# Kernel optimization log

Measured on AMD Instinct MI355X. Metric: run time of the kernel, lower is better.

The kernel has to match this reference:

```python
import jax, jax.numpy as jnp
import numpy as np

B, S, D, NH = 4, 1000, 1024, 16
DK = D // NH  # 64
NEG_INF = -jnp.inf


def setup_inputs() -> dict:
    key = jax.random.key(0)
    ks = jax.random.split(key, 12)
    sc = 1.0 / np.sqrt(D)
    inp = {
        'q': jax.random.normal(ks[0], (B, S, D), jnp.float32),
        'k': jax.random.normal(ks[1], (B, S, D), jnp.float32),
        'v': jax.random.normal(ks[2], (B, S, D), jnp.float32),
        'mask': jnp.ones((B, S), jnp.int32),
        'Wq': jax.random.normal(ks[3], (D, D), jnp.float32) * sc,
        'bq': jax.random.normal(ks[4], (D,), jnp.float32) * sc,
        'Wk': jax.random.normal(ks[5], (D, D), jnp.float32) * sc,
        'bk': jax.random.normal(ks[6], (D,), jnp.float32) * sc,
        'Wv': jax.random.normal(ks[7], (D, D), jnp.float32) * sc,
        'bv': jax.random.normal(ks[8], (D,), jnp.float32) * sc,
        'Wp': jax.random.normal(ks[9], (D, D), jnp.float32) * sc,
        'bp': jax.random.normal(ks[10], (D,), jnp.float32) * sc,
    }
    return inp


def _split_heads(x):
    # [B, S, D] -> [B, NH, S, DK]
    b, s, _ = x.shape
    return x.reshape(b, s, NH, DK).transpose(0, 2, 1, 3)


def reference(q, k, v, mask, Wq, bq, Wk, bk, Wv, bv, Wp, bp):
    # nn.Linear: y = x @ W.T + b
    Q = _split_heads(q @ Wq.T + bq)
    K = _split_heads(k @ Wk.T + bk)
    V = _split_heads(v @ Wv.T + bv)
    # scores: [B, NH, Sq, Sk]
    S_ = jnp.einsum('bhqd,bhkd->bhqk', Q, K) / jnp.sqrt(jnp.float32(DK))
    # padding mask: [B, 1, 1, Sk]
    S_ = jnp.where(mask[:, None, None, :] == 0, NEG_INF, S_)
    # causal mask (registered tril buffer sliced to [Sq, Sk])
    sq, sk = S_.shape[2], S_.shape[3]
    causal = jnp.tril(jnp.ones((sq, sk), jnp.float32))
    S_ = jnp.where(causal == 0, NEG_INF, S_)
    A = jax.nn.softmax(S_, axis=-1)  # dropout p=0 -> identity
    # context: [B, NH, Sq, DK] -> [B, Sq, D]
    x = jnp.einsum('bhqk,bhkd->bhqd', A, V).transpose(0, 2, 1, 3)
    x = x.reshape(x.shape[0], x.shape[1], -1)
    x = x @ Wp.T + bp
    return (x, A)
```

## Files before the change

kernel.cpp:

```cpp
#include <hip/hip_runtime.h>

typedef unsigned short u16;
typedef unsigned int u32;
typedef __bf16 bf16x8 __attribute__((ext_vector_type(8)));
typedef float f32x4 __attribute__((ext_vector_type(4)));
typedef u16   u16x8 __attribute__((ext_vector_type(8)));

__device__ __forceinline__ u16 f2bf(float f) {
  __bf16 b = (__bf16)f;
  return __builtin_bit_cast(u16, b);
}
__device__ __forceinline__ float bf2f(u16 u) {
  unsigned int x = ((unsigned int)u) << 16;
  return __builtin_bit_cast(float, x);
}

__device__ __forceinline__ void gll16(const u16* g, u16* l) {
  __builtin_amdgcn_global_load_lds(
      (const __attribute__((address_space(1))) void*)g,
      (__attribute__((address_space(3))) void*)l, 16, 0, 0);
}

__global__ __launch_bounds__(256) void convall_kernel(
    const float* __restrict__ s0, const float* __restrict__ s1,
    const float* __restrict__ s2, const float* __restrict__ s3,
    const float* __restrict__ s4, const float* __restrict__ s5,
    const float* __restrict__ s6,
    u16* __restrict__ o0, u16* __restrict__ o1, u16* __restrict__ o2,
    u16* __restrict__ o3, u16* __restrict__ o4, u16* __restrict__ o5,
    u16* __restrict__ o6)
{
  const int z = blockIdx.z;
  const float* s = (z == 0) ? s0 : (z == 1) ? s1 : (z == 2) ? s2 :
                   (z == 3) ? s3 : (z == 4) ? s4 : (z == 5) ? s5 : s6;
  u16* o = (z == 0) ? o0 : (z == 1) ? o1 : (z == 2) ? o2 :
           (z == 3) ? o3 : (z == 4) ? o4 : (z == 5) ? o5 : o6;
  const long n = (z < 4) ? (1l << 20) : 4096000l;
  const long i = ((long)blockIdx.x * 256 + threadIdx.x) * 8;
  if (i >= n) return;
  f32x4 a = *(const f32x4*)(s + i);
  f32x4 b = *(const f32x4*)(s + i + 4);
  u16x8 r;
#pragma unroll
  for (int e = 0; e < 4; ++e) { r[e] = f2bf(a[e]); r[e + 4] = f2bf(b[e]); }
  *(u16x8*)(o + i) = r;
}

template<int BM, int OUT_F32>
__global__ __launch_bounds__(256, 3) void gemm_swz(
    const u16* __restrict__ A0, const u16* __restrict__ A1, const u16* __restrict__ A2,
    const u16* __restrict__ B0, const u16* __restrict__ B1, const u16* __restrict__ B2,
    const float* __restrict__ g0, const float* __restrict__ g1, const float* __restrict__ g2,
    void* __restrict__ C0, void* __restrict__ C1, void* __restrict__ C2, int Mvalid)
{
  constexpr int ACH = BM / 32;
  constexpr int MI  = BM / 32;
  const int z = blockIdx.z;
  const u16* Ab = (z == 0) ? A0 : (z == 1) ? A1 : A2;
  const u16* Bw = (z == 0) ? B0 : (z == 1) ? B1 : B2;
  const float* bias = (z == 0) ? g0 : (z == 1) ? g1 : g2;
  void* Cout = (z == 0) ? C0 : (z == 1) ? C1 : C2;

  __shared__ __align__(16) u16 As[BM * 64];
  __shared__ __align__(16) u16 Bs[128 * 64];

  const int tid = threadIdx.x;
  const int wid = tid >> 6, lane = tid & 63, ln = lane & 15, lg = lane >> 4;
  const int row0 = blockIdx.x * BM, col0 = blockIdx.y * 128;
  const int wr = (wid >> 1) * (BM / 2), wc = (wid & 1) * 64;
  const int lr8 = lane >> 3;
  const int kslot = 8 * ((lane & 7) ^ lr8);

  f32x4 acc[MI][4] = {};

  for (int kt = 0; kt < 16; ++kt) {
    const int k0 = kt * 64;
    __syncthreads();
#pragma unroll
    for (int c = 0; c < ACH; ++c) {
      int base = wid * (8 * ACH) + c * 8;
      long gr = row0 + base + lr8; if (gr >= Mvalid) gr = Mvalid - 1;
      gll16(Ab + gr * 1024 + k0 + kslot, &As[base * 64]);
    }
#pragma unroll
    for (int c = 0; c < 4; ++c) {
      int base = wid * 32 + c * 8;
      gll16(Bw + (long)(col0 + base + lr8) * 1024 + k0 + kslot, &Bs[base * 64]);
    }
    __syncthreads();

#pragma unroll
    for (int kk = 0; kk < 64; kk += 32) {
      bf16x8 af[MI], bfr[4];
#pragma unroll
      for (int i = 0; i < MI; ++i) {
        int r = wr + i * 16 + ln;
        af[i] = *(const bf16x8*)&As[r * 64 + ((kk + 8 * lg) ^ ((r & 7) << 3))];
      }
#pragma unroll
      for (int j = 0; j < 4; ++j) {
        int r = wc + j * 16 + ln;
        bfr[j] = *(const bf16x8*)&Bs[r * 64 + ((kk + 8 * lg) ^ ((r & 7) << 3))];
      }
#pragma unroll
      for (int i = 0; i < MI; ++i)
#pragma unroll
        for (int j = 0; j < 4; ++j)
          acc[i][j] = __builtin_amdgcn_mfma_f32_16x16x32_bf16(af[i], bfr[j], acc[i][j], 0, 0, 0);
    }
  }

  float bj[4];
#pragma unroll
  for (int j = 0; j < 4; ++j) bj[j] = bias[col0 + wc + j * 16 + ln];
#pragma unroll
  for (int i = 0; i < MI; ++i)
#pragma unroll
    for (int j = 0; j < 4; ++j)
#pragma unroll
      for (int reg = 0; reg < 4; ++reg) {
        int r = row0 + wr + i * 16 + 4 * lg + reg;
        int c = col0 + wc + j * 16 + ln;
        if (r < Mvalid) {
          float v = acc[i][j][reg] + bj[j];
          if constexpr (OUT_F32) ((float*)Cout)[(long)r * 1024 + c] = v;
          else                   ((u16*)Cout)[(long)r * 1024 + c] = f2bf(v);
        }
      }
}

__global__ __launch_bounds__(256) void MaskedMultiheadAttention_51591147160164_kernel(
    const u16* __restrict__ Qb, const u16* __restrict__ Kb,
    const u16* __restrict__ Vb, const int* __restrict__ maskp,
    float* __restrict__ Aout, u16* __restrict__ ctx, float* __restrict__ dumpf)
{
  __shared__ __align__(16) u16 QsPs[64 * 72];
  __shared__ __align__(16) u16 Ks[2][64 * 64];
  __shared__ __align__(16) u16 Vs[64 * 72];
  __shared__ __align__(16) float Bf[1024];

  const int bh = blockIdx.y;
  const int b = bh >> 4, h = bh & 15;
  const int tid = threadIdx.x;
  const int wid = tid >> 6, lane = tid & 63, ln = lane & 15, lg = lane >> 4;

  {
    f32x4 bv;
#pragma unroll
    for (int e = 0; e < 4; ++e) {
      int ki = tid * 4 + e;
      int mv = (ki < 1000) ? maskp[b * 1000 + ki] : 0;
      bv[e] = mv ? 0.f : -1.0e30f;
    }
    *(f32x4*)&Bf[tid * 4] = bv;
  }

  const int lr8 = lane >> 3;
  const int kslot = 8 * ((lane & 7) ^ lr8);
  const long rowb = (long)b * 1000;
  const int vr = tid >> 2, vseg = tid & 3;

  for (int half = 0; half < 2; ++half) {
    const int qb = half ? (15 - blockIdx.x) : blockIdx.x;
    const int q0 = qb * 64;
    const int nkt = qb + 1;
    const int q = q0 + wid * 16 + ln;

    __syncthreads();
#pragma unroll
    for (int p = 0; p < 2; ++p) {
      int idx = p * 256 + tid;
      int r = idx >> 3, u = idx & 7;
      int tok = q0 + r; if (tok > 999) tok = 999;
      *(u16x8*)&QsPs[r * 72 + u * 8] =
          *(const u16x8*)(Qb + (long)(b * 1000 + tok) * 1024 + h * 64 + u * 8);
    }
    __syncthreads();

    bf16x8 qf0, qf1;
    {
      int r = wid * 16 + ln;
      qf0 = *(const bf16x8*)&QsPs[r * 72 +      8 * lg];
      qf1 = *(const bf16x8*)&QsPs[r * 72 + 32 + 8 * lg];
    }
    __syncthreads();

    auto stageK = [&](int buf, int kt) {
#pragma unroll
      for (int c = 0; c < 2; ++c) {
        int r = wid * 16 + c * 8;
        gll16(Kb + (rowb + kt * 64 + r + lr8) * 1024 + h * 64 + kslot, &Ks[buf][r * 64]);
      }
    };
    auto loadV = [&](int kt, u16x8& ra, u16x8& rb) {
      const u16* s = Vb + (rowb + kt * 64 + vr) * 1024 + h * 64 + vseg * 16;
      ra = *(const u16x8*)s; rb = *(const u16x8*)(s + 8);
    };
    auto writeV = [&](const u16x8& ra, const u16x8& rb) {
#pragma unroll
      for (int e = 0; e < 8; ++e) Vs[(vseg * 16 + e) * 72 + vr] = ra[e];
#pragma unroll
      for (int e = 0; e < 8; ++e) Vs[(vseg * 16 + 8 + e) * 72 + vr] = rb[e];
    };
    auto computeS = [&](int buf, f32x4 sf[4]) {
#pragma unroll
      for (int j = 0; j < 4; ++j) {
        int r = j * 16 + ln;
        int sw = (r & 7) << 3;
        bf16x8 kf0 = *(const bf16x8*)&Ks[buf][r * 64 + ((     8 * lg) ^ sw)];
        bf16x8 kf1 = *(const bf16x8*)&Ks[buf][r * 64 + ((32 + 8 * lg) ^ sw)];
        f32x4 z = {0.f, 0.f, 0.f, 0.f};
        z = __builtin_amdgcn_mfma_f32_16x16x32_bf16(kf0, qf0, z, 0, 0, 0);
        z = __builtin_amdgcn_mfma_f32_16x16x32_bf16(kf1, qf1, z, 0, 0, 0);
        sf[j] = z;
      }
    };

    float m = -3.0e38f, l = 0.f;

    stageK(0, 0); stageK(1, 1);
    for (int t = 0; t < nkt; ++t) {
      const int buf = t & 1;
      if (t == 0 || t + 1 < nkt) asm volatile("s_waitcnt vmcnt(2)" ::: "memory");
      else                       asm volatile("s_waitcnt vmcnt(0)" ::: "memory");
      __builtin_amdgcn_sched_barrier(0);
      __builtin_amdgcn_s_barrier();

      f32x4 sf[4]; computeS(buf, sf);
      float sv[4][4];
      float smax = -3.0e38f;
#pragma unroll
      for (int j = 0; j < 4; ++j) {
        int kb = t * 64 + j * 16 + 4 * lg;
        f32x4 b4 = *(const f32x4*)&Bf[kb];
#pragma unroll
        for (int reg = 0; reg < 4; ++reg) {
          float s = sf[j][reg] * 0.125f + b4[reg];
          s = (kb + reg <= q) ? s : -1.0e30f;
          sv[j][reg] = s;
          smax = fmaxf(smax, s);
        }
      }
      smax = fmaxf(smax, __shfl_xor(smax, 16));
      smax = fmaxf(smax, __shfl_xor(smax, 32));
      float mnew = fmaxf(m, smax);
      float sum = 0.f;
#pragma unroll
      for (int j = 0; j < 4; ++j)
#pragma unroll
        for (int reg = 0; reg < 4; ++reg)
          sum += __expf(sv[j][reg] - mnew);
      sum += __shfl_xor(sum, 16);
      sum += __shfl_xor(sum, 32);
      l = l * __expf(m - mnew) + sum;
      m = mnew;
      __builtin_amdgcn_s_barrier();
      if (t + 2 < nkt) stageK(buf, t + 2);
    }

    const float rl = 1.0f / l;

    f32x4 cacc[4] = {};
    u16* Pw = &QsPs[wid * 16 * 72];

    u16x8 va0, va1, vb0, vb1;
    stageK(0, 0); loadV(0, va0, va1);
    stageK(1, 1); loadV(1, vb0, vb1);
    for (int t = 0; t < nkt; ++t) {
      const int buf = t & 1;
      if (t == 0 || t + 1 == nkt) asm volatile("s_waitcnt vmcnt(4)" ::: "memory");
      else                        asm volatile("s_waitcnt vmcnt(8)" ::: "memory");
      __builtin_amdgcn_sched_barrier(0);
      if (t & 1) writeV(vb0, vb1); else writeV(va0, va1);
      asm volatile("s_waitcnt lgkmcnt(0)" ::: "memory");
      __builtin_amdgcn_sched_barrier(0);
      __builtin_amdgcn_s_barrier();

      f32x4 sf[4]; computeS(buf, sf);
      const long arow = ((long)bh * 1000 + q) * 1000;
#pragma unroll
      for (int j = 0; j < 4; ++j) {
        int kb = t * 64 + j * 16 + 4 * lg;
        f32x4 b4 = *(const f32x4*)&Bf[kb];
        f32x4 pv4;
#pragma unroll
        for (int reg = 0; reg < 4; ++reg) {
          float s = sf[j][reg] * 0.125f + b4[reg];
          s = (kb + reg <= q) ? s : -1.0e30f;
          pv4[reg] = __expf(s - m) * rl;
        }
        float* dst = (q < 1000 && kb < 1000) ? (float*)&Aout[arow + kb]
                                             : dumpf + tid * 4;
        *(f32x4*)dst = pv4;
        u32 w0 = (u32)f2bf(pv4[0]) | ((u32)f2bf(pv4[1]) << 16);
        u32 w1 = (u32)f2bf(pv4[2]) | ((u32)f2bf(pv4[3]) << 16);
        uint2 pk; pk.x = w0; pk.y = w1;
        *(uint2*)&Pw[ln * 72 + j * 16 + 4 * lg] = pk;
      }
      asm volatile("s_waitcnt lgkmcnt(0)" ::: "memory");
      __builtin_amdgcn_sched_barrier(0);
#pragma unroll
      for (int kk = 0; kk < 64; kk += 32) {
        bf16x8 pf = *(const bf16x8*)&Pw[ln * 72 + kk + 8 * lg];
#pragma unroll
        for (int jn = 0; jn < 4; ++jn) {
          bf16x8 vf = *(const bf16x8*)&Vs[(jn * 16 + ln) * 72 + kk + 8 * lg];
          cacc[jn] = __builtin_amdgcn_mfma_f32_16x16x32_bf16(pf, vf, cacc[jn], 0, 0, 0);
        }
      }
      __builtin_amdgcn_s_barrier();
      if (t + 2 < nkt) {
        stageK(buf, t + 2);
        if (t & 1) loadV(t + 2, vb0, vb1); else loadV(t + 2, va0, va1);
      }
    }
    asm volatile("s_waitcnt vmcnt(0)" ::: "memory");

    const int qrow = q0 + wid * 16 + 4 * lg;
#pragma unroll
    for (int jn = 0; jn < 4; ++jn)
#pragma unroll
      for (int reg = 0; reg < 4; ++reg) {
        int qi = qrow + reg;
        if (qi < 1000)
          ctx[(long)(b * 1000 + qi) * 1024 + h * 64 + jn * 16 + ln] = f2bf(cacc[jn][reg]);
      }
  }
}

extern "C" void kernel_launch(void* const* d_in, const int* in_sizes, int n_in,
                              void* d_out, int out_size, void* d_ws, size_t ws_size,
                              hipStream_t stream)
{
  const float* q  = (const float*)d_in[0];
  const float* k  = (const float*)d_in[1];
  const float* v  = (const float*)d_in[2];
  const int*  msk = (const int*)d_in[3];
  const float* Wq = (const float*)d_in[4];
  const float* bq = (const float*)d_in[5];
  const float* Wk = (const float*)d_in[6];
  const float* bk = (const float*)d_in[7];
  const float* Wv = (const float*)d_in[8];
  const float* bv = (const float*)d_in[9];
  const float* Wp = (const float*)d_in[10];
  const float* bp = (const float*)d_in[11];

  u16* ws  = (u16*)d_ws;
  u16* Qc  = ws;
  u16* Kc  = ws + 4096000u;
  u16* Vc  = ws + 2u * 4096000u;
  u16* Qb  = ws + 3u * 4096000u;
  u16* Kb  = ws + 4u * 4096000u;
  u16* Vb  = ws + 5u * 4096000u;
  u16* wqb = ws + 6u * 4096000u;
  u16* wkb = wqb + (1u << 20);
  u16* wvb = wkb + (1u << 20);
  u16* wpb = wvb + (1u << 20);
  float* dumpf = (float*)(wpb + (1u << 20));
  u16* ctx = Qc;

  float* Xout = (float*)d_out;
  float* Aout = Xout + 4096000;

  convall_kernel<<<dim3(2000, 1, 7), 256, 0, stream>>>(
      Wq, Wk, Wv, Wp, q, k, v,
      wqb, wkb, wvb, wpb, Qc, Kc, Vc);
  gemm_swz<128, 0><<<dim3(32, 8, 3), 256, 0, stream>>>(
      Qc, Kc, Vc, wqb, wkb, wvb, bq, bk, bv, Qb, Kb, Vb, 4000);
  MaskedMultiheadAttention_51591147160164_kernel<<<dim3(8, 64), 256, 0, stream>>>(
      Qb, Kb, Vb, msk, Aout, ctx, dumpf);
  gemm_swz<64, 1><<<dim3(63, 8, 1), 256, 0, stream>>>(
      ctx, ctx, ctx, wpb, wpb, wpb, bp, bp, bp, Xout, Xout, Xout, 4000);
}
```

Before: 143.2 us.

## Emit V projection transposed and stage V tiles via async LDS loads

The QKV projection GEMM now writes the V output in transposed [D][tokens] layout. This lets the attention kernel stage V tiles straight into a swizzled, double-buffered LDS region with global_load_lds, the same way it already stages K. It removes the per-tile register load, the scalar transposing LDS writes and an extra lgkmcnt wait from the attention loop. The cost is a strided, uncoalesced 2-byte store epilogue for the V slice of the GEMM, plus extra LDS for the second V buffer.

```diff
diff --git a/kernel.cpp b/kernel.cpp
--- a/kernel.cpp
+++ b/kernel.cpp
@@ -51,7 +51,8 @@
     const u16* __restrict__ A0, const u16* __restrict__ A1, const u16* __restrict__ A2,
     const u16* __restrict__ B0, const u16* __restrict__ B1, const u16* __restrict__ B2,
     const float* __restrict__ g0, const float* __restrict__ g1, const float* __restrict__ g2,
-    void* __restrict__ C0, void* __restrict__ C1, void* __restrict__ C2, int Mvalid)
+    void* __restrict__ C0, void* __restrict__ C1, void* __restrict__ C2,
+    int Mvalid, int tz)
 {
   constexpr int ACH = BM / 32;
   constexpr int MI  = BM / 32;
@@ -123,20 +124,24 @@
         int c = col0 + wc + j * 16 + ln;
         if (r < Mvalid) {
           float v = acc[i][j][reg] + bj[j];
-          if constexpr (OUT_F32) ((float*)Cout)[(long)r * 1024 + c] = v;
-          else                   ((u16*)Cout)[(long)r * 1024 + c] = f2bf(v);
+          if constexpr (OUT_F32) {
+            ((float*)Cout)[(long)r * 1024 + c] = v;
+          } else {
+            if (z == tz) ((u16*)Cout)[(long)c * 4000 + r] = f2bf(v);
+            else         ((u16*)Cout)[(long)r * 1024 + c] = f2bf(v);
+          }
         }
       }
 }
 
 __global__ __launch_bounds__(256) void MaskedMultiheadAttention_51591147160164_kernel(
     const u16* __restrict__ Qb, const u16* __restrict__ Kb,
-    const u16* __restrict__ Vb, const int* __restrict__ maskp,
+    const u16* __restrict__ Vt, const int* __restrict__ maskp,
     float* __restrict__ Aout, u16* __restrict__ ctx, float* __restrict__ dumpf)
 {
   __shared__ __align__(16) u16 QsPs[64 * 72];
   __shared__ __align__(16) u16 Ks[2][64 * 64];
-  __shared__ __align__(16) u16 Vs[64 * 72];
+  __shared__ __align__(16) u16 Vs[2][64 * 64];
   __shared__ __align__(16) float Bf[1024];
 
   const int bh = blockIdx.y;
@@ -158,7 +163,6 @@
   const int lr8 = lane >> 3;
   const int kslot = 8 * ((lane & 7) ^ lr8);
   const long rowb = (long)b * 1000;
-  const int vr = tid >> 2, vseg = tid & 3;
 
   for (int half = 0; half < 2; ++half) {
     const int qb = half ? (15 - blockIdx.x) : blockIdx.x;
@@ -192,15 +196,13 @@
         gll16(Kb + (rowb + kt * 64 + r + lr8) * 1024 + h * 64 + kslot, &Ks[buf][r * 64]);
       }
     };
-    auto loadV = [&](int kt, u16x8& ra, u16x8& rb) {
-      const u16* s = Vb + (rowb + kt * 64 + vr) * 1024 + h * 64 + vseg * 16;
-      ra = *(const u16x8*)s; rb = *(const u16x8*)(s + 8);
-    };
-    auto writeV = [&](const u16x8& ra, const u16x8& rb) {
-#pragma unroll
-      for (int e = 0; e < 8; ++e) Vs[(vseg * 16 + e) * 72 + vr] = ra[e];
-#pragma unroll
-      for (int e = 0; e < 8; ++e) Vs[(vseg * 16 + 8 + e) * 72 + vr] = rb[e];
+    auto stageV = [&](int buf, int kt) {
+#pragma unroll
+      for (int c = 0; c < 2; ++c) {
+        int r = wid * 16 + c * 8;
+        gll16(Vt + (long)(h * 64 + r + lr8) * 4000 + rowb + kt * 64 + kslot,
+              &Vs[buf][r * 64]);
+      }
     };
     auto computeS = [&](int buf, f32x4 sf[4]) {
 #pragma unroll
@@ -263,16 +265,12 @@
     f32x4 cacc[4] = {};
     u16* Pw = &QsPs[wid * 16 * 72];
 
-    u16x8 va0, va1, vb0, vb1;
-    stageK(0, 0); loadV(0, va0, va1);
-    stageK(1, 1); loadV(1, vb0, vb1);
+    stageK(0, 0); stageV(0, 0);
+    stageK(1, 1); stageV(1, 1);
     for (int t = 0; t < nkt; ++t) {
       const int buf = t & 1;
       if (t == 0 || t + 1 == nkt) asm volatile("s_waitcnt vmcnt(4)" ::: "memory");
       else                        asm volatile("s_waitcnt vmcnt(8)" ::: "memory");
-      __builtin_amdgcn_sched_barrier(0);
-      if (t & 1) writeV(vb0, vb1); else writeV(va0, va1);
-      asm volatile("s_waitcnt lgkmcnt(0)" ::: "memory");
       __builtin_amdgcn_sched_barrier(0);
       __builtin_amdgcn_s_barrier();
 
@@ -304,15 +302,13 @@
         bf16x8 pf = *(const bf16x8*)&Pw[ln * 72 + kk + 8 * lg];
 #pragma unroll
         for (int jn = 0; jn < 4; ++jn) {
-          bf16x8 vf = *(const bf16x8*)&Vs[(jn * 16 + ln) * 72 + kk + 8 * lg];
+          int dr = jn * 16 + ln;
+          bf16x8 vf = *(const bf16x8*)&Vs[buf][dr * 64 + ((kk + 8 * lg) ^ ((dr & 7) << 3))];
           cacc[jn] = __builtin_amdgcn_mfma_f32_16x16x32_bf16(pf, vf, cacc[jn], 0, 0, 0);
         }
       }
       __builtin_amdgcn_s_barrier();
-      if (t + 2 < nkt) {
-        stageK(buf, t + 2);
-        if (t & 1) loadV(t + 2, vb0, vb1); else loadV(t + 2, va0, va1);
-      }
+      if (t + 2 < nkt) { stageK(buf, t + 2); stageV(buf, t + 2); }
     }
     asm volatile("s_waitcnt vmcnt(0)" ::: "memory");
 
@@ -351,7 +347,7 @@
   u16* Vc  = ws + 2u * 4096000u;
   u16* Qb  = ws + 3u * 4096000u;
   u16* Kb  = ws + 4u * 4096000u;
-  u16* Vb  = ws + 5u * 4096000u;
+  u16* Vt  = ws + 5u * 4096000u;
   u16* wqb = ws + 6u * 4096000u;
   u16* wkb = wqb + (1u << 20);
   u16* wvb = wkb + (1u << 20);
@@ -366,9 +362,9 @@
       Wq, Wk, Wv, Wp, q, k, v,
       wqb, wkb, wvb, wpb, Qc, Kc, Vc);
   gemm_swz<128, 0><<<dim3(32, 8, 3), 256, 0, stream>>>(
-      Qc, Kc, Vc, wqb, wkb, wvb, bq, bk, bv, Qb, Kb, Vb, 4000);
+      Qc, Kc, Vc, wqb, wkb, wvb, bq, bk, bv, Qb, Kb, Vt, 4000, 2);
   MaskedMultiheadAttention_51591147160164_kernel<<<dim3(8, 64), 256, 0, stream>>>(
-      Qb, Kb, Vb, msk, Aout, ctx, dumpf);
+      Qb, Kb, Vt, msk, Aout, ctx, dumpf);
   gemm_swz<64, 1><<<dim3(63, 8, 1), 256, 0, stream>>>(
-      ctx, ctx, ctx, wpb, wpb, wpb, bp, bp, bp, Xout, Xout, Xout, 4000);
-}
+      ctx, ctx, ctx, wpb, wpb, wpb, bp, bp, bp, Xout, Xout, Xout, 4000, -1);
+}
```

After: 146.0 us. No clear change (+2.0%).
